# Performance work log

Measured on AMD Instinct MI355X. Metric: run time of the kernel, lower is better.

## Reference

```python
import jax, jax.numpy as jnp
import numpy as np

S, B, D = 2048, 16, 512  # seq_len, batch, dim_in (= value_dim = key_dim)


def setup_inputs() -> dict:
    key = jax.random.key(0)
    ks = jax.random.split(key, 7)
    scale = 1.0 / np.sqrt(D)
    return {
        "seq": jax.random.normal(ks[0], (S, B, D), dtype=jnp.float32),
        "Wv": jax.random.normal(ks[1], (D, D), dtype=jnp.float32) * scale,
        "bv": jax.random.normal(ks[2], (D,), dtype=jnp.float32) * 0.01,
        "Wq": jax.random.normal(ks[3], (D, D), dtype=jnp.float32) * scale,
        "bq": jax.random.normal(ks[4], (D,), dtype=jnp.float32) * 0.01,
        "Wk": jax.random.normal(ks[5], (D, D), dtype=jnp.float32) * scale,
        "bk": jax.random.normal(ks[6], (D,), dtype=jnp.float32) * 0.01,
    }


def reference(seq, Wv, bv, Wq, bq, Wk, bk):
    # seq: [S, B, D] -> [B, S, D]
    x = jnp.transpose(seq, (1, 0, 2))
    value = x @ Wv.T + bv   # [B, S, Dv]
    query = x @ Wq.T + bq   # [B, S, Dv]
    keys = x @ Wk.T + bk    # [B, S, Dk]
    inv_sqrt_d = 1.0 / np.sqrt(seq.shape[-1]).astype(np.float32)
    # note: scores use value @ query^T (roles swapped vs standard SDPA), per source
    weights = jnp.einsum('bsd,btd->bst', value, query) * inv_sqrt_d  # [B, S, S]
    weights = jax.nn.softmax(weights, axis=-1)
    out = jnp.einsum('bst,btk->bsk', weights, keys)  # [B, S, Dk]
    return jnp.transpose(out, (1, 0, 2))  # [S, B, Dk]
```

## Files before the change

### kernel.cpp

```cpp
#include <hip/hip_runtime.h>
#include <hip/hip_bf16.h>

#define SS 2048
#define BB 16
#define DD 512

typedef __attribute__((ext_vector_type(4))) float f32x4;
typedef __attribute__((ext_vector_type(8))) short bf16x8;
typedef __attribute__((ext_vector_type(4))) unsigned short us4;
typedef unsigned short us;

#define MFMA16(a,b,c) __builtin_amdgcn_mfma_f32_16x16x32_bf16((a),(b),(c),0,0,0)
#define BAR() __builtin_amdgcn_s_barrier()
#define WAITV(n) asm volatile("s_waitcnt vmcnt(" #n ")" ::: "memory")
#define WAITL()  asm volatile("s_waitcnt lgkmcnt(0)" ::: "memory")

__device__ __forceinline__ unsigned short f2b(float f) {
    union { float f; unsigned u; } v; v.f = f;
    unsigned r = v.u + 0x7FFFu + ((v.u >> 16) & 1u);
    return (unsigned short)(r >> 16);
}

__device__ __forceinline__ bf16x8 ldfrag(const us* base, int row, int kelem, int rowshift) {
    int off = (row << rowshift) + (kelem << 1);
    off ^= (row & 7) << 4;
    return *(const bf16x8*)((const char*)base + off);
}

__device__ __forceinline__ void gl16(const void* g, void* l) {
    __builtin_amdgcn_global_load_lds(
        (const __attribute__((address_space(1))) unsigned*)g,
        (__attribute__((address_space(3))) unsigned*)l, 16, 0, 0);
}

__global__ __launch_bounds__(256) void k_prep_x(const float* __restrict__ seq,
        us* __restrict__ Xb, us* __restrict__ Xbt) {
    __shared__ __align__(16) char L[64 * 128];
    const int tid = threadIdx.x;
    const int d0 = blockIdx.x * 64, s0 = blockIdx.y * 64, b = blockIdx.z;
    {
        int r = tid >> 2, seg = (tid & 3) * 16;
        const float* src = seq + (size_t)(s0 + r) * (BB * DD) + (size_t)b * DD + d0 + seg;
        __align__(16) us vals[16];
        #pragma unroll
        for (int q = 0; q < 4; ++q) {
            f32x4 v = *(const f32x4*)(src + q * 4);
            vals[q*4+0] = f2b(v.x); vals[q*4+1] = f2b(v.y);
            vals[q*4+2] = f2b(v.z); vals[q*4+3] = f2b(v.w);
        }
        us* xo = Xb + ((size_t)b * SS + s0 + r) * DD + d0 + seg;
        *(bf16x8*)xo       = *(bf16x8*)&vals[0];
        *(bf16x8*)(xo + 8) = *(bf16x8*)&vals[8];
        #pragma unroll
        for (int j = 0; j < 16; ++j) {
            int d = seg + j;
            int addr = (d * 128 + r * 2) ^ ((d & 7) << 4);
            *(us*)(L + addr) = vals[j];
        }
    }
    __syncthreads();
    {
        int d = tid >> 2, sseg = (tid & 3) * 16;
        int c = (d & 7) << 4;
        int base = d * 128 + sseg * 2;
        bf16x8 h0 = *(bf16x8*)(L + (base ^ c));
        bf16x8 h1 = *(bf16x8*)(L + ((base + 16) ^ c));
        us* o = Xbt + ((size_t)b * DD + d0 + d) * SS + s0 + sseg;
        *(bf16x8*)o       = h0;
        *(bf16x8*)(o + 8) = h1;
    }
}

__global__ __launch_bounds__(256) void k_prepG(const float* __restrict__ Wv,
        const float* __restrict__ Wq, us* __restrict__ Gt) {
    __shared__ float Sq[32][64], Sv[32][64];
    const int tid = threadIdx.x;
    const int p0 = blockIdx.x * 64, i0 = blockIdx.y * 64;
    const int tp = tid & 15, ti = tid >> 4;
    float acc[4][4] = {};
    for (int a0 = 0; a0 < DD; a0 += 32) {
        #pragma unroll
        for (int j = 0; j < 2; ++j) {
            int slot = tid + j * 256;
            int row = slot >> 4, c4 = (slot & 15) * 4;
            *(f32x4*)&Sq[row][c4] = *(const f32x4*)(Wq + (size_t)(a0 + row) * DD + p0 + c4);
            *(f32x4*)&Sv[row][c4] = *(const f32x4*)(Wv + (size_t)(a0 + row) * DD + i0 + c4);
        }
        __syncthreads();
        for (int a = 0; a < 32; ++a) {
            f32x4 q = *(f32x4*)&Sq[a][tp * 4];
            f32x4 v = *(f32x4*)&Sv[a][ti * 4];
            #pragma unroll
            for (int x = 0; x < 4; ++x)
                #pragma unroll
                for (int y = 0; y < 4; ++y)
                    acc[x][y] += q[x] * v[y];
        }
        __syncthreads();
    }
    const float sc = 0.044194173824159216f;
    #pragma unroll
    for (int x = 0; x < 4; ++x)
        #pragma unroll
        for (int y = 0; y < 4; ++y)
            Gt[(size_t)(p0 + tp * 4 + x) * DD + i0 + ti * 4 + y] = f2b(acc[x][y] * sc);
}

__global__ __launch_bounds__(512) void k_prepU(const float* __restrict__ Wq,
        const float* __restrict__ bv, float* __restrict__ u) {
    int p = threadIdx.x;
    float s = 0.f;
    for (int a0 = 0; a0 < DD; a0 += 8) {
        #pragma unroll
        for (int j = 0; j < 8; ++j)
            s += bv[a0 + j] * Wq[(size_t)(a0 + j) * DD + p];
    }
    u[p] = s * 0.044194173824159216f;
}

__global__ void k_prepW(const float* __restrict__ Wk, us* __restrict__ Wkb) {
    int i = (blockIdx.x * 256 + threadIdx.x) * 4;
    f32x4 v = *(const f32x4*)(Wk + i);
    us4 o; o.x = f2b(v.x); o.y = f2b(v.y); o.z = f2b(v.z); o.w = f2b(v.w);
    *(us4*)(Wkb + i) = o;
}

template<int OUTMODE>
__global__ __launch_bounds__(256, 2) void k_gemm(
        const us* __restrict__ A, const us* __restrict__ Bm,
        const float* __restrict__ bias, void* __restrict__ outp) {
    __shared__ __align__(16) us As[2][128 * 64];
    __shared__ __align__(16) us Bs[2][128 * 64];
    const int tid = threadIdx.x;
    const int lane = tid & 63;
    const int w = tid >> 6;
    const int wr = w >> 1, wc = w & 1;
    const int l15 = lane & 15, lg = lane >> 4;
    const int b = blockIdx.x >> 4;
    const int s0 = (blockIdx.x & 15) * 128;
    const int n0 = blockIdx.y * 128;
    const char* abase = (const char*)(A + ((size_t)b * SS + s0) * DD);
    const char* bbase = (const char*)Bm + (size_t)n0 * 1024;

    f32x4 acc[4][4];
    #pragma unroll
    for (int m = 0; m < 4; ++m)
        #pragma unroll
        for (int n = 0; n < 4; ++n) acc[m][n] = (f32x4)(0.0f);

    auto stage = [&](int db, int p) {
        #pragma unroll
        for (int j = 0; j < 4; ++j) {
            int x = (tid + j * 256) * 16;
            int gx = x ^ (((x >> 7) & 7) << 4);
            int row = gx >> 7, col = gx & 127;
            gl16(abase + (size_t)row * 1024 + p * 128 + col, (char*)As[db] + x);
            gl16(bbase + (size_t)row * 1024 + p * 128 + col, (char*)Bs[db] + x);
        }
    };

    stage(0, 0);
    for (int p = 0; p < 8; ++p) {
        if (p < 7) { stage((p + 1) & 1, p + 1); WAITV(8); }
        else       { WAITV(0); }
        BAR();
        const us* Ac = As[p & 1]; const us* Bc = Bs[p & 1];
        __builtin_amdgcn_s_setprio(1);
        #pragma unroll
        for (int kk = 0; kk < 2; ++kk) {
            bf16x8 af[4], bfr[4];
            #pragma unroll
            for (int m = 0; m < 4; ++m) af[m]  = ldfrag(Ac, 64 * wr + 16 * m + l15, kk * 32 + 8 * lg, 7);
            #pragma unroll
            for (int n = 0; n < 4; ++n) bfr[n] = ldfrag(Bc, 64 * wc + 16 * n + l15, kk * 32 + 8 * lg, 7);
            #pragma unroll
            for (int m = 0; m < 4; ++m)
                #pragma unroll
                for (int n = 0; n < 4; ++n)
                    acc[m][n] = MFMA16(af[m], bfr[n], acc[m][n]);
        }
        __builtin_amdgcn_s_setprio(0);
        BAR();
    }

    #pragma unroll
    for (int m = 0; m < 4; ++m) {
        #pragma unroll
        for (int n = 0; n < 4; ++n) {
            int col = n0 + 64 * wc + 16 * n + l15;
            float bia = bias[col];
            #pragma unroll
            for (int r = 0; r < 4; ++r) {
                int row = s0 + 64 * wr + 16 * m + 4 * lg + r;
                float v = acc[m][n][r] + bia;
                if (OUTMODE == 0)
                    ((us*)outp)[((size_t)b * SS + row) * DD + col] = f2b(v);
                else
                    ((float*)outp)[((size_t)row * BB + b) * DD + col] = v;
            }
        }
    }
}

__global__ __launch_bounds__(512, 2) void k_attn(
        const us* __restrict__ Vtb, const us* __restrict__ Xb,
        const us* __restrict__ Xbt, us* __restrict__ Ob) {
    __shared__ __align__(16) us BUFS[4][8192];
    __shared__ __align__(16) us Pb[64 * 128];
    __shared__ float red[2][2][64];

    const int tid = threadIdx.x;
    const int lane = tid & 63;
    const int w = tid >> 6;
    const int rg = w & 3;
    const int cg = w >> 2;
    const int l15 = lane & 15, lg = lane >> 4;

    const int wg = blockIdx.x;
    const int b  = wg & 15;
    const int s0 = (wg >> 4) * 64;

    const char* vbase  = (const char*)(Vtb + ((size_t)b * SS + s0) * DD);
    const char* xabase = (const char*)(Xb  + (size_t)b * SS * DD);
    const char* xtbase = (const char*)(Xbt + (size_t)b * DD * SS);

    auto issueX = [&](int kc, int tt, char* buf) {
        #pragma unroll
        for (int j = 0; j < 2; ++j) {
            int x = (tid + j * 512) * 16;
            int gx = x ^ (((x >> 7) & 7) << 4);
            int row = gx >> 7, col = gx & 127;
            gl16(xabase + (size_t)(tt + row) * 1024 + kc * 128 + col, buf + x);
        }
    };
    auto issueT = [&](int ec, int tt, char* buf) {
        #pragma unroll
        for (int j = 0; j < 2; ++j) {
            int x = (tid + j * 512) * 16;
            int gx = x ^ (((x >> 8) & 7) << 4);
            int row = gx >> 8, col = gx & 255;
            gl16(xtbase + (size_t)(ec * 64 + row) * (SS * 2) + (size_t)tt * 2 + col, buf + x);
        }
    };

    bf16x8 af[16];
    #pragma unroll
    for (int vc = 0; vc < 4; ++vc) {
        #pragma unroll
        for (int j = 0; j < 2; ++j) {
            int x = (tid + j * 512) * 16;
            int gx = x ^ (((x >> 8) & 7) << 4);
            int row = gx >> 8, col = gx & 255;
            gl16(vbase + (size_t)row * 1024 + vc * 256 + col, (char*)BUFS[vc] + x);
        }
    }
    WAITV(0); BAR();
    #pragma unroll
    for (int vc = 0; vc < 4; ++vc)
        #pragma unroll
        for (int kk = 0; kk < 4; ++kk)
            af[vc * 4 + kk] = ldfrag(BUFS[vc], 16 * rg + l15, kk * 32 + 8 * lg, 8);
    WAITL(); BAR();

    issueX(0, 0, (char*)BUFS[0]);
    issueX(1, 0, (char*)BUFS[1]);
    issueX(2, 0, (char*)BUFS[2]);

    f32x4 accv[8][2];
    #pragma unroll
    for (int ph = 0; ph < 8; ++ph)
        #pragma unroll
        for (int nt = 0; nt < 2; ++nt) accv[ph][nt] = (f32x4)(0.0f);
    float mstate[4], lstate[4];
    #pragma unroll
    for (int ri = 0; ri < 4; ++ri) { mstate[ri] = -INFINITY; lstate[ri] = 0.0f; }

    const int idx = 16 * rg + 4 * lg;

    for (int t0 = 0; t0 < SS; t0 += 128) {
        const int t0n = (t0 + 128) & (SS - 1);
        f32x4 sacc[4];
        #pragma unroll
        for (int nt = 0; nt < 4; ++nt) sacc[nt] = (f32x4)(0.0f);

        #pragma unroll
        for (int c = 0; c < 8; ++c) {
            if (c + 3 < 8) issueX(c + 3, t0, (char*)BUFS[(c + 3) & 3]);
            else           issueT(c + 3 - 8, t0, (char*)BUFS[(c + 3) & 3]);
            WAITV(6); BAR();
            const us* bufc = BUFS[c & 3];
            __builtin_amdgcn_s_setprio(1);
            #pragma unroll
            for (int kk = 0; kk < 2; ++kk) {
                #pragma unroll
                for (int nt = 0; nt < 4; ++nt) {
                    bf16x8 bq = ldfrag(bufc, 64 * cg + 16 * nt + l15, kk * 32 + 8 * lg, 7);
                    sacc[nt] = MFMA16(af[2 * c + kk], bq, sacc[nt]);
                }
            }
            __builtin_amdgcn_s_setprio(0);
            BAR();
        }

        float rmax[4], alpha[4], rsum[4];
        #pragma unroll
        for (int ri = 0; ri < 4; ++ri) {
            float v = fmaxf(fmaxf(sacc[0][ri], sacc[1][ri]), fmaxf(sacc[2][ri], sacc[3][ri]));
            #pragma unroll
            for (int d = 1; d < 16; d <<= 1) v = fmaxf(v, __shfl_xor(v, d));
            rmax[ri] = v;
            if (l15 == 0) red[0][cg][idx + ri] = v;
        }
        WAITL(); BAR();
        #pragma unroll
        for (int ri = 0; ri < 4; ++ri) {
            float mn = fmaxf(mstate[ri], fmaxf(rmax[ri], red[0][cg ^ 1][idx + ri]));
            alpha[ri] = __expf(mstate[ri] - mn);
            mstate[ri] = mn;
        }
        #pragma unroll
        for (int nt = 0; nt < 4; ++nt)
            #pragma unroll
            for (int ri = 0; ri < 4; ++ri)
                sacc[nt][ri] = __expf(sacc[nt][ri] - mstate[ri]);
        #pragma unroll
        for (int ri = 0; ri < 4; ++ri) {
            float s = sacc[0][ri] + sacc[1][ri] + sacc[2][ri] + sacc[3][ri];
            #pragma unroll
            for (int d = 1; d < 16; d <<= 1) s += __shfl_xor(s, d);
            rsum[ri] = s;
            if (l15 == 0) red[1][cg][idx + ri] = s;
        }
        #pragma unroll
        for (int nt = 0; nt < 4; ++nt)
            #pragma unroll
            for (int ri = 0; ri < 4; ++ri) {
                int row = idx + ri;
                int col = 64 * cg + 16 * nt + l15;
                int off = ((row << 8) + (col << 1)) ^ ((row & 7) << 4);
                *(us*)((char*)Pb + off) = f2b(sacc[nt][ri]);
            }
        #pragma unroll
        for (int ph = 0; ph < 8; ++ph)
            #pragma unroll
            for (int nt = 0; nt < 2; ++nt)
                #pragma unroll
                for (int ri = 0; ri < 4; ++ri)
                    accv[ph][nt][ri] *= alpha[ri];
        #pragma unroll
        for (int ri = 0; ri < 4; ++ri) lstate[ri] *= alpha[ri];
        WAITL(); BAR();
        #pragma unroll
        for (int ri = 0; ri < 4; ++ri)
            lstate[ri] += rsum[ri] + red[1][cg ^ 1][idx + ri];

        #pragma unroll
        for (int c = 8; c < 16; ++c) {
            if (c + 3 < 16) issueT(c + 3 - 8, t0, (char*)BUFS[(c + 3) & 3]);
            else            issueX(c + 3 - 16, t0n, (char*)BUFS[(c + 3) & 3]);
            WAITV(6); BAR();
            const us* bufc = BUFS[c & 3];
            const int ph = c - 8;
            __builtin_amdgcn_s_setprio(1);
            #pragma unroll
            for (int kk = 0; kk < 4; ++kk) {
                bf16x8 pa = ldfrag(Pb, 16 * rg + l15, kk * 32 + 8 * lg, 8);
                #pragma unroll
                for (int nt = 0; nt < 2; ++nt) {
                    bf16x8 bx = ldfrag(bufc, 32 * cg + 16 * nt + l15, kk * 32 + 8 * lg, 8);
                    accv[ph][nt] = MFMA16(pa, bx, accv[ph][nt]);
                }
            }
            __builtin_amdgcn_s_setprio(0);
            BAR();
        }
    }

    us* orow = Ob + ((size_t)b * SS + s0) * DD;
    #pragma unroll
    for (int ph = 0; ph < 8; ++ph)
        #pragma unroll
        for (int nt = 0; nt < 2; ++nt)
            #pragma unroll
            for (int ri = 0; ri < 4; ++ri) {
                int row = idx + ri;
                int e = 64 * ph + 32 * cg + 16 * nt + l15;
                orow[(size_t)row * DD + e] = f2b(accv[ph][nt][ri] / lstate[ri]);
            }
}

extern "C" void kernel_launch(void* const* d_in, const int* in_sizes, int n_in,
                              void* d_out, int out_size, void* d_ws, size_t ws_size,
                              hipStream_t stream) {
    const float* seq = (const float*)d_in[0];
    const float* Wv  = (const float*)d_in[1];
    const float* bv  = (const float*)d_in[2];
    const float* Wq  = (const float*)d_in[3];
    const float* Wk  = (const float*)d_in[5];
    const float* bk  = (const float*)d_in[6];

    char* ws = (char*)d_ws;
    us*    Xb  = (us*)ws;
    us*    Xbt = (us*)(ws + (size_t)33554432);
    us*    Vtb = (us*)(ws + (size_t)67108864);
    us*    Gt  = (us*)(ws + (size_t)100663296);
    us*    Wkb = (us*)(ws + (size_t)101187584);
    float* u   = (float*)(ws + (size_t)101711872);

    k_prep_x<<<dim3(8, 32, 16), 256, 0, stream>>>(seq, Xb, Xbt);
    k_prepG<<<dim3(8, 8), 256, 0, stream>>>(Wv, Wq, Gt);
    k_prepU<<<1, 512, 0, stream>>>(Wq, bv, u);
    k_prepW<<<256, 256, 0, stream>>>(Wk, Wkb);

    k_gemm<0><<<dim3(256, 4), 256, 0, stream>>>(Xb, Gt, u, (void*)Vtb);
    k_attn<<<512, 512, 0, stream>>>(Vtb, Xb, Xbt, Vtb);
    k_gemm<1><<<dim3(256, 4), 256, 0, stream>>>(Vtb, Wkb, bk, d_out);
}
```

Before: 403.1 us.

## Widen attention key tiles to 256, use 3-slot 32KB ring, drop online max

Restructures the attention kernel to process 256 keys per step. It uses a 2x4 wave grid in which each wave computes two 16-row fragments, so each loaded B-fragment feeds two MFMAs. The load pipeline becomes a 3-slot ring of 32KB tiles with new XOR swizzles. The online-softmax running max and rescaling are removed: scores are exponentiated directly and the row sums are reduced once at the end. This avoids per-step cross-wave max reductions and accumulator rescaling, but it relies on scores staying small enough not to overflow exp. LDS use also roughly doubles, which may stop two blocks from fitting per CU.

```diff
diff --git a/kernel.cpp b/kernel.cpp
--- a/kernel.cpp
+++ b/kernel.cpp
@@ -14,6 +14,7 @@
 #define BAR() __builtin_amdgcn_s_barrier()
 #define WAITV(n) asm volatile("s_waitcnt vmcnt(" #n ")" ::: "memory")
 #define WAITL()  asm volatile("s_waitcnt lgkmcnt(0)" ::: "memory")
+#define ADV(s) s = ((s) == 2 ? 0 : (s) + 1)
 
 __device__ __forceinline__ unsigned short f2b(float f) {
     union { float f; unsigned u; } v; v.f = f;
@@ -21,6 +22,16 @@
     return (unsigned short)(r >> 16);
 }
 
+__device__ __forceinline__ bf16x8 ldfrag9(const us* base, int row, int kelem) {
+    int off = (row << 9) + (kelem << 1);
+    off ^= (row & 15) << 5;
+    return *(const bf16x8*)((const char*)base + off);
+}
+__device__ __forceinline__ bf16x8 ldfrag8(const us* base, int row, int kelem) {
+    int off = (row << 8) + (kelem << 1);
+    off ^= ((row & 3) << 6) ^ (((row >> 2) & 1) << 4);
+    return *(const bf16x8*)((const char*)base + off);
+}
 __device__ __forceinline__ bf16x8 ldfrag(const us* base, int row, int kelem, int rowshift) {
     int off = (row << rowshift) + (kelem << 1);
     off ^= (row & 7) << 4;
@@ -205,15 +216,15 @@
 __global__ __launch_bounds__(512, 2) void k_attn(
         const us* __restrict__ Vtb, const us* __restrict__ Xb,
         const us* __restrict__ Xbt, us* __restrict__ Ob) {
-    __shared__ __align__(16) us BUFS[4][8192];
-    __shared__ __align__(16) us Pb[64 * 128];
-    __shared__ float red[2][2][64];
+    __shared__ __align__(16) us BUFS[3][16384];
+    __shared__ __align__(16) us Pb[64 * 256];
+    __shared__ float red[4][64];
 
     const int tid = threadIdx.x;
     const int lane = tid & 63;
     const int w = tid >> 6;
-    const int rg = w & 3;
-    const int cg = w >> 2;
+    const int rg = w & 1;
+    const int cg = w >> 1;
     const int l15 = lane & 15, lg = lane >> 4;
 
     const int wg = blockIdx.x;
@@ -224,169 +235,180 @@
     const char* xabase = (const char*)(Xb  + (size_t)b * SS * DD);
     const char* xtbase = (const char*)(Xbt + (size_t)b * DD * SS);
 
-    auto issueX = [&](int kc, int tt, char* buf) {
-        #pragma unroll
-        for (int j = 0; j < 2; ++j) {
-            int x = (tid + j * 512) * 16;
-            int gx = x ^ (((x >> 7) & 7) << 4);
-            int row = gx >> 7, col = gx & 127;
-            gl16(xabase + (size_t)(tt + row) * 1024 + kc * 128 + col, buf + x);
+    auto issue = [&](int cflat, int slot) {
+        int c = cflat & 127;
+        int i = c & 15, t0 = (c >> 4) << 8;
+        char* dst = (char*)BUFS[slot];
+        if (i < 8) {
+            #pragma unroll
+            for (int j = 0; j < 4; ++j) {
+                int x = tid * 16 + j * 8192;
+                int gx = x ^ (((x >> 9) & 15) << 5);
+                int row = gx >> 9, col = gx & 511;
+                gl16(xabase + (size_t)(t0 + 64 * (i & 3) + row) * 1024 + (i >> 2) * 512 + col, dst + x);
+            }
+        } else {
+            #pragma unroll
+            for (int j = 0; j < 4; ++j) {
+                int x = tid * 16 + j * 8192;
+                int gx = x ^ (((x >> 8) & 3) << 6) ^ (((x >> 10) & 1) << 4);
+                int row = gx >> 8, col = gx & 255;
+                gl16(xtbase + (size_t)(128 * (i & 3) + row) * 4096
+                            + (size_t)(t0 + 128 * ((i >> 2) & 1)) * 2 + col, dst + x);
+            }
         }
     };
-    auto issueT = [&](int ec, int tt, char* buf) {
-        #pragma unroll
-        for (int j = 0; j < 2; ++j) {
-            int x = (tid + j * 512) * 16;
-            int gx = x ^ (((x >> 8) & 7) << 4);
-            int row = gx >> 8, col = gx & 255;
-            gl16(xtbase + (size_t)(ec * 64 + row) * (SS * 2) + (size_t)tt * 2 + col, buf + x);
-        }
-    };
-
-    bf16x8 af[16];
-    #pragma unroll
-    for (int vc = 0; vc < 4; ++vc) {
-        #pragma unroll
-        for (int j = 0; j < 2; ++j) {
-            int x = (tid + j * 512) * 16;
-            int gx = x ^ (((x >> 8) & 7) << 4);
-            int row = gx >> 8, col = gx & 255;
-            gl16(vbase + (size_t)row * 1024 + vc * 256 + col, (char*)BUFS[vc] + x);
+
+    #pragma unroll
+    for (int vc = 0; vc < 2; ++vc) {
+        #pragma unroll
+        for (int j = 0; j < 4; ++j) {
+            int x = tid * 16 + j * 8192;
+            int gx = x ^ (((x >> 9) & 15) << 5);
+            int row = gx >> 9, col = gx & 511;
+            gl16(vbase + (size_t)row * 1024 + vc * 512 + col, (char*)BUFS[vc] + x);
         }
     }
     WAITV(0); BAR();
-    #pragma unroll
-    for (int vc = 0; vc < 4; ++vc)
-        #pragma unroll
-        for (int kk = 0; kk < 4; ++kk)
-            af[vc * 4 + kk] = ldfrag(BUFS[vc], 16 * rg + l15, kk * 32 + 8 * lg, 8);
+    bf16x8 af[2][16];
+    #pragma unroll
+    for (int vc = 0; vc < 2; ++vc)
+        #pragma unroll
+        for (int ks = 0; ks < 8; ++ks) {
+            af[0][8 * vc + ks] = ldfrag9(BUFS[vc], 32 * rg + l15,      ks * 32 + 8 * lg);
+            af[1][8 * vc + ks] = ldfrag9(BUFS[vc], 32 * rg + 16 + l15, ks * 32 + 8 * lg);
+        }
     WAITL(); BAR();
 
-    issueX(0, 0, (char*)BUFS[0]);
-    issueX(1, 0, (char*)BUFS[1]);
-    issueX(2, 0, (char*)BUFS[2]);
-
-    f32x4 accv[8][2];
-    #pragma unroll
-    for (int ph = 0; ph < 8; ++ph)
-        #pragma unroll
-        for (int nt = 0; nt < 2; ++nt) accv[ph][nt] = (f32x4)(0.0f);
-    float mstate[4], lstate[4];
-    #pragma unroll
-    for (int ri = 0; ri < 4; ++ri) { mstate[ri] = -INFINITY; lstate[ri] = 0.0f; }
-
-    const int idx = 16 * rg + 4 * lg;
-
-    for (int t0 = 0; t0 < SS; t0 += 128) {
-        const int t0n = (t0 + 128) & (SS - 1);
-        f32x4 sacc[4];
-        #pragma unroll
-        for (int nt = 0; nt < 4; ++nt) sacc[nt] = (f32x4)(0.0f);
-
-        #pragma unroll
-        for (int c = 0; c < 8; ++c) {
-            if (c + 3 < 8) issueX(c + 3, t0, (char*)BUFS[(c + 3) & 3]);
-            else           issueT(c + 3 - 8, t0, (char*)BUFS[(c + 3) & 3]);
-            WAITV(6); BAR();
-            const us* bufc = BUFS[c & 3];
+    issue(0, 2); issue(1, 0);
+    int wslot = 1, rslot = 2;
+
+    f32x4 accv[4][2][2];
+    #pragma unroll
+    for (int ec = 0; ec < 4; ++ec)
+        #pragma unroll
+        for (int nt = 0; nt < 2; ++nt)
+            #pragma unroll
+            for (int rf = 0; rf < 2; ++rf) accv[ec][nt][rf] = (f32x4)(0.0f);
+    float lsum[2][4];
+    #pragma unroll
+    for (int rf = 0; rf < 2; ++rf)
+        #pragma unroll
+        for (int ri = 0; ri < 4; ++ri) lsum[rf][ri] = 0.0f;
+
+    for (int step = 0; step < 8; ++step) {
+        const int base = step * 16;
+        f32x4 sacc[2][4];
+        #pragma unroll
+        for (int rf = 0; rf < 2; ++rf)
+            #pragma unroll
+            for (int tq = 0; tq < 4; ++tq) sacc[rf][tq] = (f32x4)(0.0f);
+
+        #pragma unroll
+        for (int i = 0; i < 8; ++i) {
+            issue(base + i + 2, wslot); ADV(wslot);
+            WAITV(8); BAR();
+            const us* sl = BUFS[rslot]; ADV(rslot);
+            const int tq = i & 3, kh = i >> 2;
             __builtin_amdgcn_s_setprio(1);
             #pragma unroll
-            for (int kk = 0; kk < 2; ++kk) {
-                #pragma unroll
-                for (int nt = 0; nt < 4; ++nt) {
-                    bf16x8 bq = ldfrag(bufc, 64 * cg + 16 * nt + l15, kk * 32 + 8 * lg, 7);
-                    sacc[nt] = MFMA16(af[2 * c + kk], bq, sacc[nt]);
-                }
+            for (int ks = 0; ks < 8; ++ks) {
+                bf16x8 bq = ldfrag9(sl, 16 * cg + l15, ks * 32 + 8 * lg);
+                sacc[0][tq] = MFMA16(af[0][8 * kh + ks], bq, sacc[0][tq]);
+                sacc[1][tq] = MFMA16(af[1][8 * kh + ks], bq, sacc[1][tq]);
             }
             __builtin_amdgcn_s_setprio(0);
             BAR();
         }
 
-        float rmax[4], alpha[4], rsum[4];
-        #pragma unroll
-        for (int ri = 0; ri < 4; ++ri) {
-            float v = fmaxf(fmaxf(sacc[0][ri], sacc[1][ri]), fmaxf(sacc[2][ri], sacc[3][ri]));
-            #pragma unroll
-            for (int d = 1; d < 16; d <<= 1) v = fmaxf(v, __shfl_xor(v, d));
-            rmax[ri] = v;
-            if (l15 == 0) red[0][cg][idx + ri] = v;
-        }
+        #pragma unroll
+        for (int rf = 0; rf < 2; ++rf)
+            #pragma unroll
+            for (int tq = 0; tq < 4; ++tq)
+                #pragma unroll
+                for (int ri = 0; ri < 4; ++ri)
+                    sacc[rf][tq][ri] = __expf(sacc[rf][tq][ri]);
+        #pragma unroll
+        for (int rf = 0; rf < 2; ++rf)
+            #pragma unroll
+            for (int tq = 0; tq < 4; ++tq)
+                #pragma unroll
+                for (int ri = 0; ri < 4; ++ri) {
+                    int row = 32 * rg + 16 * rf + 4 * lg + ri;
+                    int col = 64 * tq + 16 * cg + l15;
+                    int off = ((row << 9) + (col << 1)) ^ ((row & 15) << 5);
+                    *(us*)((char*)Pb + off) = f2b(sacc[rf][tq][ri]);
+                }
+        #pragma unroll
+        for (int rf = 0; rf < 2; ++rf)
+            #pragma unroll
+            for (int ri = 0; ri < 4; ++ri) {
+                float s = sacc[rf][0][ri] + sacc[rf][1][ri] + sacc[rf][2][ri] + sacc[rf][3][ri];
+                s += __shfl_xor(s, 1); s += __shfl_xor(s, 2);
+                s += __shfl_xor(s, 4); s += __shfl_xor(s, 8);
+                lsum[rf][ri] += s;
+            }
         WAITL(); BAR();
-        #pragma unroll
-        for (int ri = 0; ri < 4; ++ri) {
-            float mn = fmaxf(mstate[ri], fmaxf(rmax[ri], red[0][cg ^ 1][idx + ri]));
-            alpha[ri] = __expf(mstate[ri] - mn);
-            mstate[ri] = mn;
-        }
-        #pragma unroll
-        for (int nt = 0; nt < 4; ++nt)
-            #pragma unroll
-            for (int ri = 0; ri < 4; ++ri)
-                sacc[nt][ri] = __expf(sacc[nt][ri] - mstate[ri]);
-        #pragma unroll
-        for (int ri = 0; ri < 4; ++ri) {
-            float s = sacc[0][ri] + sacc[1][ri] + sacc[2][ri] + sacc[3][ri];
-            #pragma unroll
-            for (int d = 1; d < 16; d <<= 1) s += __shfl_xor(s, d);
-            rsum[ri] = s;
-            if (l15 == 0) red[1][cg][idx + ri] = s;
-        }
-        #pragma unroll
-        for (int nt = 0; nt < 4; ++nt)
-            #pragma unroll
-            for (int ri = 0; ri < 4; ++ri) {
-                int row = idx + ri;
-                int col = 64 * cg + 16 * nt + l15;
-                int off = ((row << 8) + (col << 1)) ^ ((row & 7) << 4);
-                *(us*)((char*)Pb + off) = f2b(sacc[nt][ri]);
-            }
-        #pragma unroll
-        for (int ph = 0; ph < 8; ++ph)
-            #pragma unroll
-            for (int nt = 0; nt < 2; ++nt)
-                #pragma unroll
-                for (int ri = 0; ri < 4; ++ri)
-                    accv[ph][nt][ri] *= alpha[ri];
-        #pragma unroll
-        for (int ri = 0; ri < 4; ++ri) lstate[ri] *= alpha[ri];
-        WAITL(); BAR();
-        #pragma unroll
-        for (int ri = 0; ri < 4; ++ri)
-            lstate[ri] += rsum[ri] + red[1][cg ^ 1][idx + ri];
-
-        #pragma unroll
-        for (int c = 8; c < 16; ++c) {
-            if (c + 3 < 16) issueT(c + 3 - 8, t0, (char*)BUFS[(c + 3) & 3]);
-            else            issueX(c + 3 - 16, t0n, (char*)BUFS[(c + 3) & 3]);
-            WAITV(6); BAR();
-            const us* bufc = BUFS[c & 3];
-            const int ph = c - 8;
+
+        bf16x8 pa[2][4];
+        #pragma unroll
+        for (int j = 0; j < 8; ++j) {
+            if ((j & 3) == 0) {
+                const int th = j >> 2;
+                #pragma unroll
+                for (int rf = 0; rf < 2; ++rf)
+                    #pragma unroll
+                    for (int ts = 0; ts < 4; ++ts)
+                        pa[rf][ts] = ldfrag9(Pb, 32 * rg + 16 * rf + l15,
+                                             (4 * th + ts) * 32 + 8 * lg);
+            }
+            issue(base + 10 + j, wslot); ADV(wslot);
+            WAITV(8); BAR();
+            const us* sl = BUFS[rslot]; ADV(rslot);
+            const int ec = j & 3;
             __builtin_amdgcn_s_setprio(1);
             #pragma unroll
-            for (int kk = 0; kk < 4; ++kk) {
-                bf16x8 pa = ldfrag(Pb, 16 * rg + l15, kk * 32 + 8 * lg, 8);
+            for (int ts = 0; ts < 4; ++ts)
                 #pragma unroll
                 for (int nt = 0; nt < 2; ++nt) {
-                    bf16x8 bx = ldfrag(bufc, 32 * cg + 16 * nt + l15, kk * 32 + 8 * lg, 8);
-                    accv[ph][nt] = MFMA16(pa, bx, accv[ph][nt]);
+                    bf16x8 bx = ldfrag8(sl, 32 * cg + 16 * nt + l15, ts * 32 + 8 * lg);
+                    accv[ec][nt][0] = MFMA16(pa[0][ts], bx, accv[ec][nt][0]);
+                    accv[ec][nt][1] = MFMA16(pa[1][ts], bx, accv[ec][nt][1]);
                 }
-            }
             __builtin_amdgcn_s_setprio(0);
             BAR();
         }
     }
 
+    if (l15 == 0) {
+        #pragma unroll
+        for (int rf = 0; rf < 2; ++rf)
+            #pragma unroll
+            for (int ri = 0; ri < 4; ++ri)
+                red[cg][32 * rg + 16 * rf + 4 * lg + ri] = lsum[rf][ri];
+    }
+    WAITL(); BAR();
+    float tot[2][4];
+    #pragma unroll
+    for (int rf = 0; rf < 2; ++rf)
+        #pragma unroll
+        for (int ri = 0; ri < 4; ++ri) {
+            int row = 32 * rg + 16 * rf + 4 * lg + ri;
+            tot[rf][ri] = red[0][row] + red[1][row] + red[2][row] + red[3][row];
+        }
     us* orow = Ob + ((size_t)b * SS + s0) * DD;
     #pragma unroll
-    for (int ph = 0; ph < 8; ++ph)
+    for (int ec = 0; ec < 4; ++ec)
         #pragma unroll
         for (int nt = 0; nt < 2; ++nt)
             #pragma unroll
-            for (int ri = 0; ri < 4; ++ri) {
-                int row = idx + ri;
-                int e = 64 * ph + 32 * cg + 16 * nt + l15;
-                orow[(size_t)row * DD + e] = f2b(accv[ph][nt][ri] / lstate[ri]);
-            }
+            for (int rf = 0; rf < 2; ++rf)
+                #pragma unroll
+                for (int ri = 0; ri < 4; ++ri) {
+                    int row = 32 * rg + 16 * rf + 4 * lg + ri;
+                    int e = 128 * ec + 32 * cg + 16 * nt + l15;
+                    orow[(size_t)row * DD + e] = f2b(accv[ec][nt][rf][ri] / tot[rf][ri]);
+                }
 }
 
 extern "C" void kernel_launch(void* const* d_in, const int* in_sizes, int n_in,
```

After: 660.6 us. +63.9%, slower.
